# Performance work log

Hardware: AMD Instinct MI355X
Metric: run time of the kernel (lower is better)

## Reference

```python
import jax, jax.numpy as jnp
import numpy as np

D_MODEL = 1024
N_HEADS = 16
THETA = 10000.0


def _rope(x, token_positions):
    # x: (b, h, s, d_k); token_positions: (b, s)
    d_k = x.shape[-1]
    powers = jnp.arange(0, d_k, 2, dtype=jnp.float32) / d_k        # (d_k/2,)
    freqs = 1.0 / (THETA ** powers)
    ang = token_positions.astype(jnp.float32)[..., None] * freqs   # (b, s, d_k/2)
    cos = jnp.cos(ang)[:, None, :, :].astype(x.dtype)              # (b, 1, s, d_k/2)
    sin = jnp.sin(ang)[:, None, :, :].astype(x.dtype)
    x_even = x[..., ::2]
    x_odd = x[..., 1::2]
    r1 = x_even * cos - x_odd * sin
    r2 = x_even * sin + x_odd * cos
    # interleave back to (..., d_k)
    return jnp.stack([r1, r2], axis=-1).reshape(x.shape)


def reference(x, token_positions, wq, wk, wv, wo):
    B, S, D = x.shape
    H = N_HEADS
    d_k = D // H

    def proj(w):
        y = jnp.einsum('bsi,oi->bso', x, w)
        return y.reshape(B, S, H, d_k).transpose(0, 2, 1, 3)  # (b, h, s, d_k)

    q = _rope(proj(wq), token_positions)
    k = _rope(proj(wk), token_positions)
    v = proj(wv)

    scale = 1.0 / jnp.sqrt(jnp.asarray(d_k, dtype=x.dtype))
    score = jnp.einsum('bhqd,bhkd->bhqk', q, k) * scale  # (b, h, s, s)
    causal = jnp.tril(jnp.ones((S, S), dtype=bool))
    score = jnp.where(causal, score, -jnp.inf)
    probs = jax.nn.softmax(score, axis=-1)
    attn = jnp.einsum('bhqk,bhkd->bhqd', probs, v)
    attn = attn.transpose(0, 2, 1, 3).reshape(B, S, D)
    return jnp.einsum('bsi,oi->bso', attn, wo)


def setup_inputs() -> dict:
    key = jax.random.key(0)
    ks = jax.random.split(key, 6)
    B, S, D = 2, 2048, D_MODEL
    std = (2.0 / (D + D)) ** 0.5
    x = jax.random.normal(ks[0], (B, S, D), dtype=jnp.float32)
    token_positions = jnp.broadcast_to(jnp.arange(S, dtype=jnp.int32), (B, S))
    wq = jax.random.normal(ks[1], (D, D), dtype=jnp.float32) * std
    wk = jax.random.normal(ks[2], (D, D), dtype=jnp.float32) * std
    wv = jax.random.normal(ks[3], (D, D), dtype=jnp.float32) * std
    wo = jax.random.normal(ks[4], (D, D), dtype=jnp.float32) * std
    return {"x": x, "token_positions": token_positions, "wq": wq, "wk": wk, "wv": wv, "wo": wo}
```

## Files before the change

### kernel.cpp

```cpp
#include <hip/hip_runtime.h>
#include <hip/hip_bf16.h>

typedef unsigned short u16;
typedef unsigned int u32;
typedef short short8 __attribute__((ext_vector_type(8)));
typedef u16 u16x8 __attribute__((ext_vector_type(8)));
typedef u16 u16x4 __attribute__((ext_vector_type(4)));
typedef u32 u32x4 __attribute__((ext_vector_type(4)));
typedef float f32x4 __attribute__((ext_vector_type(4)));
typedef float f32x16 __attribute__((ext_vector_type(16)));

#define MFMA(a, b, c) __builtin_amdgcn_mfma_f32_16x16x32_bf16((a), (b), (c), 0, 0, 0)
#define MFMA32(a, b, c) __builtin_amdgcn_mfma_f32_32x32x16_bf16((a), (b), (c), 0, 0, 0)

#define QSCALE 0.18033688011112042f

__device__ __forceinline__ u16 f2bf(float f) {
  unsigned u = __float_as_uint(f);
  unsigned r = (u + 0x7fffu + ((u >> 16) & 1u)) >> 16;
  return (u16)r;
}
__device__ __forceinline__ float bf2f(u16 h) {
  return __uint_as_float(((unsigned)h) << 16);
}
__device__ __forceinline__ float exp2hw(float x) {
  float r;
  asm("v_exp_f32 %0, %1" : "=v"(r) : "v"(x));
  return r;
}
__device__ __forceinline__ u32 cvtpk(float lo, float hi) {
  u32 d;
  asm("v_cvt_pk_bf16_f32 %0, %1, %2" : "=v"(d) : "v"(lo), "v"(hi));
  return d;
}
__device__ __forceinline__ float max3f(float a, float b, float c) {
  float d;
  asm("v_max3_f32 %0, %1, %2, %3" : "=v"(d) : "v"(a), "v"(b), "v"(c));
  return d;
}
__device__ __forceinline__ void plswap(u32& a, u32& b) {
  asm volatile("v_permlane32_swap_b32 %0, %1" : "+v"(a), "+v"(b));
}
__device__ __forceinline__ void async16(const void* g, void* l) {
  __builtin_amdgcn_global_load_lds(
      (const __attribute__((address_space(1))) void*)g,
      (__attribute__((address_space(3))) void*)l, 16, 0, 0);
}
__device__ __forceinline__ f32x16 zero16() {
  f32x16 z;
#pragma unroll
  for (int i = 0; i < 16; i++) z[i] = 0.f;
  return z;
}
#define WAITV(N) asm volatile("s_waitcnt vmcnt(" #N ")" ::: "memory")
#define WAITL0() asm volatile("s_waitcnt lgkmcnt(0)" ::: "memory")
#define BAR() __builtin_amdgcn_s_barrier()
#define PRIO1 __builtin_amdgcn_s_setprio(1)
#define PRIO0 __builtin_amdgcn_s_setprio(0)

__global__ __launch_bounds__(256) void convert_kernel(
    const float* __restrict__ x, const float* __restrict__ wq,
    const float* __restrict__ wk, const float* __restrict__ wv,
    const float* __restrict__ wo, u16* __restrict__ ws,
    const int* __restrict__ tp, float* __restrict__ tab) {
  int blk = blockIdx.x;
  if (blk >= 4096) {
    int t = (blk - 4096) * 256 + threadIdx.x;
    int bs = t >> 5, p = t & 31;
    float freq = exp2hw(-(float)p * 0.4152410118609203f);
    float ang = (float)tp[bs] * freq;
    float sn, cs;
    sincosf(ang, &sn, &cs);
    tab[bs * 64 + p * 2] = cs;
    tab[bs * 64 + p * 2 + 1] = sn;
    return;
  }
  const float* src; u16* dst;
  if (blk < 2048)      { src = x;  dst = ws; }
  else if (blk < 2560) { src = wq; dst = ws + 4194304;               blk -= 2048; }
  else if (blk < 3072) { src = wk; dst = ws + 4194304 + 1048576;     blk -= 2560; }
  else if (blk < 3584) { src = wv; dst = ws + 4194304 + 2 * 1048576; blk -= 3072; }
  else                 { src = wo; dst = ws + 4194304 + 3 * 1048576; blk -= 3584; }
  int idx = (blk * 256 + threadIdx.x) * 8;
  float4 v0 = *(const float4*)(src + idx);
  float4 v1 = *(const float4*)(src + idx + 4);
  u16x8 o;
  o[0] = f2bf(v0.x); o[1] = f2bf(v0.y); o[2] = f2bf(v0.z); o[3] = f2bf(v0.w);
  o[4] = f2bf(v1.x); o[5] = f2bf(v1.y); o[6] = f2bf(v1.z); o[7] = f2bf(v1.w);
  *(u16x8*)(dst + idx) = o;
}

__global__ __launch_bounds__(512, 2) void gemm_qkv256(
    const u16* __restrict__ xb, const u16* __restrict__ Wg,
    const float* __restrict__ tab, u16* __restrict__ qb, u16* __restrict__ kb,
    u16* __restrict__ vt) {
  __shared__ u16 As[2][16384];
  __shared__ u16 Bs[2][12288];
  const int tid = threadIdx.x, lane = tid & 63, wid = tid >> 6;
  const int wm = wid >> 2, wn = wid & 3;
  const int g = lane >> 4, r = lane & 15;
  const int lid = ((blockIdx.x & 7) << 5) + (blockIdx.x >> 3);
  const int rowBase = (lid >> 4) << 8;
  const int colBase = (lid & 15) * 192;

#define STG_A(BUF, T)                                                         \
  do {                                                                        \
    _Pragma("unroll") for (int i_ = 0; i_ < 4; ++i_) {                        \
      int c = i_ * 512 + tid;                                                 \
      int row = c >> 3, kc = ((c & 7) ^ (row & 7)) * 8;                       \
      async16(xb + (size_t)(rowBase + row) * 1024 + (T)*64 + kc,              \
              (char*)As[BUF] + c * 16);                                       \
    }                                                                         \
  } while (0)
#define STG_B(BUF, T)                                                         \
  do {                                                                        \
    _Pragma("unroll") for (int i_ = 0; i_ < 3; ++i_) {                        \
      int c = i_ * 512 + tid;                                                 \
      int row = c >> 3, kc = ((c & 7) ^ (row & 7)) * 8;                       \
      async16(Wg + (size_t)(colBase + row) * 1024 + (T)*64 + kc,              \
              (char*)Bs[BUF] + c * 16);                                       \
    }                                                                         \
  } while (0)

  f32x4 acc[8][3];
#pragma unroll
  for (int m = 0; m < 8; m++)
#pragma unroll
    for (int n = 0; n < 3; n++) acc[m][n] = (f32x4){0.f, 0.f, 0.f, 0.f};
  short8 af[4][2], bfr[3][2];

#define RD_A(CUR, MH)                                                         \
  do {                                                                        \
    _Pragma("unroll") for (int mi = 0; mi < 4; mi++) {                        \
      int ra = wm * 128 + (MH)*64 + mi * 16 + r;                              \
      const u16* p = As[CUR] + ra * 64;                                       \
      int sw = (ra & 7) << 3;                                                 \
      af[mi][0] = *(const short8*)(p + ((g << 3) ^ sw));                      \
      af[mi][1] = *(const short8*)(p + (((4 + g) << 3) ^ sw));                \
    }                                                                         \
  } while (0)
#define RD_B(CUR)                                                             \
  do {                                                                        \
    _Pragma("unroll") for (int ni = 0; ni < 3; ni++) {                        \
      int cb = wn * 48 + ni * 16 + r;                                         \
      const u16* p = Bs[CUR] + cb * 64;                                       \
      int sw = (cb & 7) << 3;                                                 \
      bfr[ni][0] = *(const short8*)(p + ((g << 3) ^ sw));                     \
      bfr[ni][1] = *(const short8*)(p + (((4 + g) << 3) ^ sw));               \
    }                                                                         \
  } while (0)
#define MM24(MH)                                                              \
  do {                                                                        \
    _Pragma("unroll") for (int mi = 0; mi < 4; mi++)                          \
        _Pragma("unroll") for (int ni = 0; ni < 3; ni++) {                    \
      acc[(MH)*4 + mi][ni] = MFMA(af[mi][0], bfr[ni][0], acc[(MH)*4 + mi][ni]); \
      acc[(MH)*4 + mi][ni] = MFMA(af[mi][1], bfr[ni][1], acc[(MH)*4 + mi][ni]); \
    }                                                                         \
  } while (0)

  STG_A(0, 0); STG_B(0, 0);
  STG_A(1, 1);
  WAITV(4);
  BAR();

  for (int t = 0; t < 16; ++t) {
    const int cur = t & 1, nxt = cur ^ 1;
    RD_A(cur, 0);
    RD_B(cur);
    if (t < 15) STG_B(nxt, t + 1);
    BAR(); WAITL0();
    PRIO1; MM24(0); PRIO0; BAR();
    RD_A(cur, 1);
    if (t < 14) {
      STG_A(cur, t + 2);
      WAITV(4);
    } else {
      WAITV(0);
    }
    BAR(); WAITL0();
    PRIO1; MM24(1); PRIO0; BAR();
  }
#undef STG_A
#undef STG_B
#undef RD_A
#undef RD_B
#undef MM24

  const int colF = colBase + wn * 48;
#pragma unroll
  for (int n = 0; n < 3; n++) {
    const int col3 = colF + n * 16 + r;
    const int z = col3 >> 10;
    const int col = col3 & 1023;
    if (z < 2) {
      u16* dst = z ? kb : qb;
      const float qs = z ? 1.0f : QSCALE;
      const int p2 = (col >> 1) & 31;
      const bool odd = col & 1;
#pragma unroll
      for (int m = 0; m < 8; m++)
#pragma unroll
        for (int i = 0; i < 4; i++) {
          const int row = rowBase + wm * 128 + m * 16 + g * 4 + i;
          float2 cssn = *(const float2*)(tab + row * 64 + p2 * 2);
          float v = acc[m][n][i];
          float part = __shfl_xor(v, 1);
          float res = odd ? (part * cssn.y + v * cssn.x)
                          : (v * cssn.x - part * cssn.y);
          dst[(size_t)row * 1024 + col] = f2bf(res * qs);
        }
    } else {
#pragma unroll
      for (int m = 0; m < 8; m++)
#pragma unroll
        for (int i = 0; i < 4; i++) {
          const int row = rowBase + wm * 128 + m * 16 + g * 4 + i;
          const int bb = row >> 11, s = row & 2047;
          vt[(size_t)((bb * 16 + (col >> 6)) * 64 + (col & 63)) * 2048 + s] =
              f2bf(acc[m][n][i]);
        }
    }
  }
}

__global__ __launch_bounds__(256, 4) void attn_kernel(
    const u16* __restrict__ qg, const u16* __restrict__ kg,
    const u16* __restrict__ vt, u16* __restrict__ p0, u16* __restrict__ p1,
    float* __restrict__ mbuf, float* __restrict__ lbuf) {
  __shared__ u16 Ks[2][64 * 64];
  __shared__ u16 Vs[2][64 * 64];
  const int tid = threadIdx.x, wid = tid >> 6, lane = tid & 63;
  const int q5 = lane & 31, hi = lane >> 5;
  const int akc = blockIdx.x >> 5, bh = blockIdx.x & 31;
  const int a = akc >> 2, k = (akc >> 1) & 1, c = akc & 1;
  const int b = bh >> 4, h = bh & 15;
  const int base = (wid < 2) ? a : (15 - a);
  const int rb = base * 128 + k * 64 + (wid & 1) * 32;
  const int cmax = rb >> 5;
  const int jend = 30 - 2 * a + k;
  const int qrow = (b << 11) + rb + q5;

  short8 bq[4];
  {
    const u16* qp = qg + (size_t)qrow * 1024 + (h << 6) + hi * 8;
    bq[0] = *(const short8*)(qp);
    bq[1] = *(const short8*)(qp + 16);
    bq[2] = *(const short8*)(qp + 32);
    bq[3] = *(const short8*)(qp + 48);
  }
  f32x16 accO0 = zero16(), accO1 = zero16();
  float m_r = -1e30f, l_r = 0.f;

#define STAGE(JT, BUF)                                                        \
  do {                                                                        \
    _Pragma("unroll") for (int i_ = 0; i_ < 2; i_++) {                        \
      int cc_ = i_ * 256 + tid;                                               \
      int row = cc_ >> 3, cc = (cc_ & 7) ^ (row & 7);                         \
      async16(kg + (size_t)((b << 11) + ((JT) << 6) + row) * 1024 +           \
                  (h << 6) + cc * 8,                                          \
              (char*)Ks[BUF] + cc_ * 16);                                     \
      async16(vt + (size_t)((bh << 6) + row) * 2048 + ((JT) << 6) + cc * 8,   \
              (char*)Vs[BUF] + cc_ * 16);                                     \
    }                                                                         \
  } while (0)

  if (c <= jend) STAGE(c, 0);

  for (int jj = c; jj <= jend; jj += 2) {
    const int cur = ((jj - c) >> 1) & 1;
    if (jj + 2 <= jend) {
      STAGE(jj + 2, cur ^ 1);
      WAITV(4);
    } else {
      WAITV(0);
    }
    BAR();
    if (2 * jj <= cmax) {
      const u16* Kb = Ks[cur];
      const u16* Vb = Vs[cur];
      const bool has1 = (2 * jj + 1 <= cmax);
      const int rsw = (q5 & 7) << 3;
      f32x16 s0 = zero16(), s1 = zero16();
      PRIO1;
#pragma unroll
      for (int kk = 0; kk < 4; kk++) {
        short8 kf =
            *(const short8*)(Kb + q5 * 64 + ((((kk << 1) + hi) << 3) ^ rsw));
        s0 = MFMA32(kf, bq[kk], s0);
      }
      PRIO0;
      if (has1) {
        PRIO1;
#pragma unroll
        for (int kk = 0; kk < 4; kk++) {
          short8 kf = *(const short8*)(Kb + (32 + q5) * 64 +
                                       ((((kk << 1) + hi) << 3) ^ rsw));
          s1 = MFMA32(kf, bq[kk], s1);
        }
        PRIO0;
      }
      if (2 * jj == cmax) {
#pragma unroll
        for (int rg = 0; rg < 16; rg++) {
          int rowk = (rg & 3) + 8 * (rg >> 2) + 4 * hi;
          if (rowk > q5) s0[rg] = -1e30f;
        }
      } else if (2 * jj + 1 == cmax) {
#pragma unroll
        for (int rg = 0; rg < 16; rg++) {
          int rowk = (rg & 3) + 8 * (rg >> 2) + 4 * hi;
          if (rowk > q5) s1[rg] = -1e30f;
        }
      }
      float pmax = max3f(s0[0], s0[1], s0[2]);
#pragma unroll
      for (int rg = 3; rg < 15; rg += 2) pmax = max3f(pmax, s0[rg], s0[rg + 1]);
      pmax = fmaxf(pmax, s0[15]);
      if (has1) {
#pragma unroll
        for (int rg = 0; rg < 16; rg += 2) pmax = max3f(pmax, s1[rg], s1[rg + 1]);
      }
      pmax = fmaxf(pmax, __shfl_xor(pmax, 32));
      if (!__all(pmax <= m_r + 8.0f)) {
        float mn = fmaxf(m_r, pmax);
        float sc = exp2hw(m_r - mn);
        l_r *= sc;
#pragma unroll
        for (int rg = 0; rg < 16; rg++) {
          accO0[rg] *= sc;
          accO1[rg] *= sc;
        }
        m_r = mn;
      }
      float rs = 0.f;
      u32 pw00[4], pw01[4], pw10[4], pw11[4];
#define PACK(SREG, OUT, S16)                                                  \
  do {                                                                        \
    float pp0 = exp2hw(SREG[(S16)*8 + 0] - m_r);                              \
    float pp1 = exp2hw(SREG[(S16)*8 + 1] - m_r);                              \
    float pp2 = exp2hw(SREG[(S16)*8 + 2] - m_r);                              \
    float pp3 = exp2hw(SREG[(S16)*8 + 3] - m_r);                              \
    float pp4 = exp2hw(SREG[(S16)*8 + 4] - m_r);                              \
    float pp5 = exp2hw(SREG[(S16)*8 + 5] - m_r);                              \
    float pp6 = exp2hw(SREG[(S16)*8 + 6] - m_r);                              \
    float pp7 = exp2hw(SREG[(S16)*8 + 7] - m_r);                              \
    rs += ((pp0 + pp1) + (pp2 + pp3)) + ((pp4 + pp5) + (pp6 + pp7));          \
    u32 X = cvtpk(pp0, pp1), Y = cvtpk(pp2, pp3);                             \
    u32 U = cvtpk(pp4, pp5), W = cvtpk(pp6, pp7);                             \
    plswap(X, U);                                                             \
    plswap(Y, W);                                                             \
    OUT[0] = X; OUT[1] = Y; OUT[2] = U; OUT[3] = W;                           \
  } while (0)
      PACK(s0, pw00, 0);
      PACK(s0, pw01, 1);
      if (has1) {
        PACK(s1, pw10, 0);
        PACK(s1, pw11, 1);
      }
#undef PACK
      rs += __shfl_xor(rs, 32);
      l_r += rs;
#define PVSTEP(PW, CH)                                                        \
  do {                                                                        \
    u32x4 pv_ = {PW[0], PW[1], PW[2], PW[3]};                                 \
    short8 pb_ = __builtin_bit_cast(short8, pv_);                             \
    short8 v0_ =                                                              \
        *(const short8*)(Vb + q5 * 64 + ((((CH) + hi) << 3) ^ rsw));          \
    short8 v1_ = *(const short8*)(Vb + (32 + q5) * 64 +                       \
                                  ((((CH) + hi) << 3) ^ rsw));                \
    accO0 = MFMA32(v0_, pb_, accO0);                                          \
    accO1 = MFMA32(v1_, pb_, accO1);                                          \
  } while (0)
      PRIO1;
      PVSTEP(pw00, 0);
      PVSTEP(pw01, 2);
      if (has1) {
        PVSTEP(pw10, 4);
        PVSTEP(pw11, 6);
      }
      PRIO0;
#undef PVSTEP
    }
    WAITL0();
    BAR();
  }
#undef STAGE

  u16* pout = c ? p1 : p0;
#pragma unroll
  for (int qd = 0; qd < 4; qd++) {
    u16x4 o0, o1;
#pragma unroll
    for (int e = 0; e < 4; e++) {
      o0[e] = f2bf(accO0[qd * 4 + e]);
      o1[e] = f2bf(accO1[qd * 4 + e]);
    }
    u16* op = pout + (size_t)qrow * 1024 + (h << 6) + qd * 8 + hi * 4;
    *(u16x4*)(op) = o0;
    *(u16x4*)(op + 32) = o1;
  }
  if (hi == 0) {
    int mli = c * 65536 + (bh << 11) + rb + q5;
    mbuf[mli] = m_r;
    lbuf[mli] = l_r;
  }
}

__global__ __launch_bounds__(256) void attn_merge(const u16* __restrict__ p1,
                                                  const float* __restrict__ mbuf,
                                                  const float* __restrict__ lbuf,
                                                  u16* __restrict__ ab) {
  int t = blockIdx.x * 256 + threadIdx.x;
  int dg = t & 7, row = t >> 3;
  int bh = row >> 11, s = row & 2047;
  int b = bh >> 4, h = bh & 15;
  size_t addr = (size_t)((b << 11) + s) * 1024 + (h << 6) + dg * 8;
  float m0 = mbuf[row], m1 = mbuf[65536 + row];
  float l0 = lbuf[row], l1 = lbuf[65536 + row];
  float m = fmaxf(m0, m1);
  float w0 = exp2hw(m0 - m), w1 = exp2hw(m1 - m);
  float inv = 1.0f / (l0 * w0 + l1 * w1);
  u16x8 o0 = *(const u16x8*)(ab + addr);
  u16x8 o1 = *(const u16x8*)(p1 + addr);
  u16x8 o;
#pragma unroll
  for (int i = 0; i < 8; i++)
    o[i] = f2bf((bf2f(o0[i]) * w0 + bf2f(o1[i]) * w1) * inv);
  *(u16x8*)(ab + addr) = o;
}

__global__ __launch_bounds__(512) void gemm_ao(const u16* __restrict__ ab,
                                               const u16* __restrict__ wob,
                                               float* __restrict__ out) {
  __shared__ u16 As[2][8192], Bs[2][8192];
  const int tid = threadIdx.x, lane = tid & 63, wid = tid >> 6;
  const int wm = wid >> 2, wn = wid & 3;
  const int g = lane >> 4, r = lane & 15;
  const int lid = ((blockIdx.x & 7) << 5) + (blockIdx.x >> 3);
  const int rowBase = (lid >> 3) << 7;
  const int colBase = (lid & 7) << 7;

#define AOSTG(KT, BUF)                                                        \
  do {                                                                        \
    _Pragma("unroll") for (int i_ = 0; i_ < 2; ++i_) {                        \
      int c = i_ * 512 + tid;                                                 \
      int row = c >> 3, kc = ((c & 7) ^ (row & 7)) * 8;                       \
      async16(ab + (size_t)(rowBase + row) * 1024 + ((KT) << 6) + kc,         \
              (char*)As[BUF] + c * 16);                                       \
    }                                                                         \
    _Pragma("unroll") for (int i_ = 0; i_ < 2; ++i_) {                        \
      int c = i_ * 512 + tid;                                                 \
      int row = c >> 3, kc = ((c & 7) ^ (row & 7)) * 8;                       \
      async16(wob + (size_t)(colBase + row) * 1024 + ((KT) << 6) + kc,        \
              (char*)Bs[BUF] + c * 16);                                       \
    }                                                                         \
  } while (0)

  f32x4 acc[4][2];
#pragma unroll
  for (int m = 0; m < 4; m++)
#pragma unroll
    for (int n = 0; n < 2; n++) acc[m][n] = (f32x4){0.f, 0.f, 0.f, 0.f};

  AOSTG(0, 0);
  for (int kt = 0; kt < 16; ++kt) {
    const int cur = kt & 1;
    if (kt + 1 < 16) {
      AOSTG(kt + 1, cur ^ 1);
      WAITV(4);
    } else {
      WAITV(0);
    }
    BAR();
    const u16* Ab = As[cur];
    const u16* Bb = Bs[cur];
    short8 af[4][2], bfr[2][2];
#pragma unroll
    for (int m = 0; m < 4; m++) {
      int ra = wm * 64 + m * 16 + r;
      const u16* p = Ab + ra * 64;
      int sw = (ra & 7) << 3;
      af[m][0] = *(const short8*)(p + ((g << 3) ^ sw));
      af[m][1] = *(const short8*)(p + (((4 + g) << 3) ^ sw));
    }
#pragma unroll
    for (int n = 0; n < 2; n++) {
      int cb = wn * 32 + n * 16 + r;
      const u16* p = Bb + cb * 64;
      int sw = (cb & 7) << 3;
      bfr[n][0] = *(const short8*)(p + ((g << 3) ^ sw));
      bfr[n][1] = *(const short8*)(p + (((4 + g) << 3) ^ sw));
    }
    PRIO1;
#pragma unroll
    for (int m = 0; m < 4; m++)
#pragma unroll
      for (int n = 0; n < 2; n++) {
        acc[m][n] = MFMA(af[m][0], bfr[n][0], acc[m][n]);
        acc[m][n] = MFMA(af[m][1], bfr[n][1], acc[m][n]);
      }
    PRIO0;
    WAITL0();
    BAR();
  }
#undef AOSTG

  const int rowB = rowBase + wm * 64;
  const int colB = colBase + wn * 32;
#pragma unroll
  for (int m = 0; m < 4; m++)
#pragma unroll
    for (int n = 0; n < 2; n++)
#pragma unroll
      for (int i = 0; i < 4; i++)
        out[(size_t)(rowB + m * 16 + g * 4 + i) * 1024 + colB + n * 16 + r] =
            acc[m][n][i];
}

extern "C" void kernel_launch(void* const* d_in, const int* in_sizes, int n_in,
                              void* d_out, int out_size, void* d_ws,
                              size_t ws_size, hipStream_t stream) {
  const float* x = (const float*)d_in[0];
  const int* tp = (const int*)d_in[1];
  const float* wq = (const float*)d_in[2];
  const float* wk = (const float*)d_in[3];
  const float* wv = (const float*)d_in[4];
  const float* wo = (const float*)d_in[5];
  float* out = (float*)d_out;

  u16* ws = (u16*)d_ws;
  u16* xb = ws;
  u16* wqb = xb + 4194304;
  u16* wkb = wqb + 1048576;
  u16* wvb = wkb + 1048576;
  u16* wob = wvb + 1048576;
  u16* qb = wob + 1048576;
  u16* kb = qb + 4194304;
  u16* vtb = kb + 4194304;
  u16* ab = vtb + 4194304;
  float* tab = (float*)ab;
  float* mbuf = (float*)wqb;
  float* lbuf = (float*)wkb;

  convert_kernel<<<4608, 256, 0, stream>>>(x, wq, wk, wv, wo, ws, tp, tab);
  gemm_qkv256<<<256, 512, 0, stream>>>(xb, wqb, tab, qb, kb, vtb);
  attn_kernel<<<1024, 256, 0, stream>>>(qb, kb, vtb, ab, xb, mbuf, lbuf);
  attn_merge<<<2048, 256, 0, stream>>>(xb, mbuf, lbuf, ab);
  gemm_ao<<<256, 512, 0, stream>>>(ab, wob, out);
}
```

Before: 104.7 us.

## Fuse split-KV attention merge into output projection GEMM A-tile load

Replaces the separate attn_merge pass with a small wprep kernel that precomputes per-row merge weights, folding the normalisation into those weights. gemm_ao now loads both partial attention outputs through registers, blends them with the weights, and writes the merged bf16 tile into shared memory, overlapped with the MFMA work on the current buffer. This removes the full read-modify-write of the attention buffer and one large launch. In exchange the A operand no longer uses async global-to-LDS copies, which adds register pressure, VALU work and load latency inside the GEMM loop.

```diff
diff --git a/kernel.cpp b/kernel.cpp
--- a/kernel.cpp
+++ b/kernel.cpp
@@ -406,30 +406,21 @@
   }
 }
 
-__global__ __launch_bounds__(256) void attn_merge(const u16* __restrict__ p1,
-                                                  const float* __restrict__ mbuf,
-                                                  const float* __restrict__ lbuf,
-                                                  u16* __restrict__ ab) {
-  int t = blockIdx.x * 256 + threadIdx.x;
-  int dg = t & 7, row = t >> 3;
-  int bh = row >> 11, s = row & 2047;
-  int b = bh >> 4, h = bh & 15;
-  size_t addr = (size_t)((b << 11) + s) * 1024 + (h << 6) + dg * 8;
-  float m0 = mbuf[row], m1 = mbuf[65536 + row];
-  float l0 = lbuf[row], l1 = lbuf[65536 + row];
+__global__ __launch_bounds__(256) void wprep(const float* __restrict__ mbuf,
+                                             const float* __restrict__ lbuf,
+                                             float2* __restrict__ wbuf) {
+  int i = blockIdx.x * 256 + threadIdx.x;
+  float m0 = mbuf[i], m1 = mbuf[65536 + i];
+  float l0 = lbuf[i], l1 = lbuf[65536 + i];
   float m = fmaxf(m0, m1);
   float w0 = exp2hw(m0 - m), w1 = exp2hw(m1 - m);
   float inv = 1.0f / (l0 * w0 + l1 * w1);
-  u16x8 o0 = *(const u16x8*)(ab + addr);
-  u16x8 o1 = *(const u16x8*)(p1 + addr);
-  u16x8 o;
-#pragma unroll
-  for (int i = 0; i < 8; i++)
-    o[i] = f2bf((bf2f(o0[i]) * w0 + bf2f(o1[i]) * w1) * inv);
-  *(u16x8*)(ab + addr) = o;
-}
-
-__global__ __launch_bounds__(512) void gemm_ao(const u16* __restrict__ ab,
+  wbuf[i] = make_float2(w0 * inv, w1 * inv);
+}
+
+__global__ __launch_bounds__(512) void gemm_ao(const u16* __restrict__ p0,
+                                               const u16* __restrict__ p1,
+                                               const float2* __restrict__ wbuf,
                                                const u16* __restrict__ wob,
                                                float* __restrict__ out) {
   __shared__ u16 As[2][8192], Bs[2][8192];
@@ -440,21 +431,39 @@
   const int rowBase = (lid >> 3) << 7;
   const int colBase = (lid & 7) << 7;
 
-#define AOSTG(KT, BUF)                                                        \
+  const int c0 = tid, c1 = tid + 512;
+  const int r0 = c0 >> 3, kc0 = ((c0 & 7) ^ (r0 & 7)) * 8;
+  const int r1 = c1 >> 3, kc1 = ((c1 & 7) ^ (r1 & 7)) * 8;
+  const int grow0 = rowBase + r0, grow1 = rowBase + r1;
+  const int b0 = grow0 >> 11, s0 = grow0 & 2047;
+  const int b1 = grow1 >> 11, s1 = grow1 & 2047;
+
+#define B_STG(BUF, T)                                                         \
   do {                                                                        \
     _Pragma("unroll") for (int i_ = 0; i_ < 2; ++i_) {                        \
       int c = i_ * 512 + tid;                                                 \
       int row = c >> 3, kc = ((c & 7) ^ (row & 7)) * 8;                       \
-      async16(ab + (size_t)(rowBase + row) * 1024 + ((KT) << 6) + kc,         \
-              (char*)As[BUF] + c * 16);                                       \
-    }                                                                         \
-    _Pragma("unroll") for (int i_ = 0; i_ < 2; ++i_) {                        \
-      int c = i_ * 512 + tid;                                                 \
-      int row = c >> 3, kc = ((c & 7) ^ (row & 7)) * 8;                       \
-      async16(wob + (size_t)(colBase + row) * 1024 + ((KT) << 6) + kc,        \
+      async16(wob + (size_t)(colBase + row) * 1024 + ((T) << 6) + kc,         \
               (char*)Bs[BUF] + c * 16);                                       \
     }                                                                         \
   } while (0)
+#define A_LOAD(T)                                                             \
+  u16x8 a00 = *(const u16x8*)(p0 + (size_t)grow0 * 1024 + ((T) << 6) + kc0);  \
+  u16x8 a10 = *(const u16x8*)(p1 + (size_t)grow0 * 1024 + ((T) << 6) + kc0);  \
+  u16x8 a01 = *(const u16x8*)(p0 + (size_t)grow1 * 1024 + ((T) << 6) + kc1);  \
+  u16x8 a11 = *(const u16x8*)(p1 + (size_t)grow1 * 1024 + ((T) << 6) + kc1);  \
+  float2 W0v = wbuf[(size_t)(((b0 << 4) + (T)) << 11) + s0];                  \
+  float2 W1v = wbuf[(size_t)(((b1 << 4) + (T)) << 11) + s1]
+#define A_MERGE(BUF)                                                          \
+  do {                                                                        \
+    u16x8 o0_, o1_;                                                           \
+    _Pragma("unroll") for (int e_ = 0; e_ < 8; e_++) {                        \
+      o0_[e_] = f2bf(bf2f(a00[e_]) * W0v.x + bf2f(a10[e_]) * W0v.y);          \
+      o1_[e_] = f2bf(bf2f(a01[e_]) * W1v.x + bf2f(a11[e_]) * W1v.y);          \
+    }                                                                         \
+    *(u16x8*)((char*)As[BUF] + c0 * 16) = o0_;                                \
+    *(u16x8*)((char*)As[BUF] + c1 * 16) = o1_;                                \
+  } while (0)
 
   f32x4 acc[4][2];
 #pragma unroll
@@ -462,48 +471,85 @@
 #pragma unroll
     for (int n = 0; n < 2; n++) acc[m][n] = (f32x4){0.f, 0.f, 0.f, 0.f};
 
-  AOSTG(0, 0);
-  for (int kt = 0; kt < 16; ++kt) {
-    const int cur = kt & 1;
-    if (kt + 1 < 16) {
-      AOSTG(kt + 1, cur ^ 1);
-      WAITV(4);
+  {
+    A_LOAD(0);
+    B_STG(0, 0);
+    A_MERGE(0);
+  }
+  WAITL0();
+
+  for (int t = 0; t < 16; ++t) {
+    const int cur = t & 1, nxt = cur ^ 1;
+    WAITV(0);
+    BAR();
+    if (t < 15) {
+      A_LOAD(t + 1);
+      B_STG(nxt, t + 1);
+      const u16* Ab = As[cur];
+      const u16* Bb = Bs[cur];
+      short8 af[4][2], bfr[2][2];
+#pragma unroll
+      for (int m = 0; m < 4; m++) {
+        int ra = wm * 64 + m * 16 + r;
+        const u16* p = Ab + ra * 64;
+        int sw = (ra & 7) << 3;
+        af[m][0] = *(const short8*)(p + ((g << 3) ^ sw));
+        af[m][1] = *(const short8*)(p + (((4 + g) << 3) ^ sw));
+      }
+#pragma unroll
+      for (int n = 0; n < 2; n++) {
+        int cb = wn * 32 + n * 16 + r;
+        const u16* p = Bb + cb * 64;
+        int sw = (cb & 7) << 3;
+        bfr[n][0] = *(const short8*)(p + ((g << 3) ^ sw));
+        bfr[n][1] = *(const short8*)(p + (((4 + g) << 3) ^ sw));
+      }
+      PRIO1;
+#pragma unroll
+      for (int m = 0; m < 4; m++)
+#pragma unroll
+        for (int n = 0; n < 2; n++) {
+          acc[m][n] = MFMA(af[m][0], bfr[n][0], acc[m][n]);
+          acc[m][n] = MFMA(af[m][1], bfr[n][1], acc[m][n]);
+        }
+      PRIO0;
+      A_MERGE(nxt);
     } else {
-      WAITV(0);
+      const u16* Ab = As[cur];
+      const u16* Bb = Bs[cur];
+      short8 af[4][2], bfr[2][2];
+#pragma unroll
+      for (int m = 0; m < 4; m++) {
+        int ra = wm * 64 + m * 16 + r;
+        const u16* p = Ab + ra * 64;
+        int sw = (ra & 7) << 3;
+        af[m][0] = *(const short8*)(p + ((g << 3) ^ sw));
+        af[m][1] = *(const short8*)(p + (((4 + g) << 3) ^ sw));
+      }
+#pragma unroll
+      for (int n = 0; n < 2; n++) {
+        int cb = wn * 32 + n * 16 + r;
+        const u16* p = Bb + cb * 64;
+        int sw = (cb & 7) << 3;
+        bfr[n][0] = *(const short8*)(p + ((g << 3) ^ sw));
+        bfr[n][1] = *(const short8*)(p + (((4 + g) << 3) ^ sw));
+      }
+      PRIO1;
+#pragma unroll
+      for (int m = 0; m < 4; m++)
+#pragma unroll
+        for (int n = 0; n < 2; n++) {
+          acc[m][n] = MFMA(af[m][0], bfr[n][0], acc[m][n]);
+          acc[m][n] = MFMA(af[m][1], bfr[n][1], acc[m][n]);
+        }
+      PRIO0;
     }
-    BAR();
-    const u16* Ab = As[cur];
-    const u16* Bb = Bs[cur];
-    short8 af[4][2], bfr[2][2];
-#pragma unroll
-    for (int m = 0; m < 4; m++) {
-      int ra = wm * 64 + m * 16 + r;
-      const u16* p = Ab + ra * 64;
-      int sw = (ra & 7) << 3;
-      af[m][0] = *(const short8*)(p + ((g << 3) ^ sw));
-      af[m][1] = *(const short8*)(p + (((4 + g) << 3) ^ sw));
-    }
-#pragma unroll
-    for (int n = 0; n < 2; n++) {
-      int cb = wn * 32 + n * 16 + r;
-      const u16* p = Bb + cb * 64;
-      int sw = (cb & 7) << 3;
-      bfr[n][0] = *(const short8*)(p + ((g << 3) ^ sw));
-      bfr[n][1] = *(const short8*)(p + (((4 + g) << 3) ^ sw));
-    }
-    PRIO1;
-#pragma unroll
-    for (int m = 0; m < 4; m++)
-#pragma unroll
-      for (int n = 0; n < 2; n++) {
-        acc[m][n] = MFMA(af[m][0], bfr[n][0], acc[m][n]);
-        acc[m][n] = MFMA(af[m][1], bfr[n][1], acc[m][n]);
-      }
-    PRIO0;
     WAITL0();
     BAR();
   }
-#undef AOSTG
+#undef B_STG
+#undef A_LOAD
+#undef A_MERGE
 
   const int rowB = rowBase + wm * 64;
   const int colB = colBase + wn * 32;
@@ -541,10 +587,11 @@
   float* tab = (float*)ab;
   float* mbuf = (float*)wqb;
   float* lbuf = (float*)wkb;
+  float2* wbuf = (float2*)wvb;
 
   convert_kernel<<<4608, 256, 0, stream>>>(x, wq, wk, wv, wo, ws, tp, tab);
   gemm_qkv256<<<256, 512, 0, stream>>>(xb, wqb, tab, qb, kb, vtb);
   attn_kernel<<<1024, 256, 0, stream>>>(qb, kb, vtb, ab, xb, mbuf, lbuf);
-  attn_merge<<<2048, 256, 0, stream>>>(xb, mbuf, lbuf, ab);
-  gemm_ao<<<256, 512, 0, stream>>>(ab, wob, out);
-}
+  wprep<<<256, 256, 0, stream>>>(mbuf, lbuf, wbuf);
+  gemm_ao<<<256, 512, 0, stream>>>(ab, xb, wbuf, wob, out);
+}
```

Measured after the change: 113.9 us. +8.8%, slower.
